# Kernel optimization log

Measured on AMD Instinct MI355X. Metric: run time of the kernel, lower is better.

The kernel has to match this reference:

```python
import jax, jax.numpy as jnp
import numpy as np

SIGMA = 20.0  # outlier threshold from FindOutliers


def setup_inputs() -> dict:
    key = jax.random.key(0)
    k1, k2, k3 = jax.random.split(key, 3)
    B, S, K, N = 4, 2048, 4096, 4096
    x = jax.random.normal(k1, (B, S, K), dtype=jnp.float32).astype(jnp.float16)
    # inject outlier columns (every 512th column scaled up) so |x| > sigma fires,
    # exercising the mixed sparse(outlier)/dense int8 decomposition
    x = (x.astype(jnp.float32).at[..., ::512].multiply(40.0)).astype(jnp.float16)
    weight = (jax.random.normal(k2, (N, K), dtype=jnp.float32) * 0.02).astype(jnp.float16)
    bias = (jax.random.normal(k3, (N,), dtype=jnp.float32) * 0.01).astype(jnp.float16)
    return {"x": x, "weight": weight, "bias": bias}


def reference(x, weight, bias):
    # x: [B, S, K] fp16; weight: [N, K] fp16; bias: [N] fp16
    B, S, K = x.shape
    N = weight.shape[0]
    xf = x.astype(jnp.float32).reshape(-1, K)            # [M, K]
    w32 = weight.astype(jnp.float32)                     # [N, K]

    # FindOutliers: columns of the flattened activation with any |value| > sigma
    out_mask = jnp.any(jnp.abs(xf) > SIGMA, axis=0)      # [K] bool

    # weight quantization: zero outlier columns, per-output-row symmetric int8 scale
    w_base = jnp.where(out_mask[None, :], 0.0, w32)      # [N, K]
    scale_col = (jnp.max(jnp.abs(w_base), axis=1) / 127.0).astype(jnp.float16).astype(jnp.float32)
    scale_col = jnp.maximum(scale_col, 1e-8)             # guard all-zero rows
    q_w = jnp.round(jnp.clip(w_base / scale_col[:, None], -128.0, 127.0)).astype(jnp.int8)

    # FindRowScaleF32: per-row symmetric int8 quantization of the activation
    scale_row = jnp.max(jnp.abs(xf), axis=1, keepdims=True) / 127.0   # [M, 1] fp32
    scale_row = jnp.maximum(scale_row, 1e-8)
    q_x = jnp.round(jnp.clip(xf / scale_row, -128.0, 127.0)).astype(jnp.int8)

    # int8 GEMM with int32 accumulation, fused dequant epilogue
    acc = jax.lax.dot_general(q_x, q_w, (((1,), (1,)), ((), ())),
                              preferred_element_type=jnp.int32)      # [M, N]
    y = acc.astype(jnp.float32) * scale_row * scale_col[None, :]

    # sparse outlier part in fp16-precision math: x[:, ind] @ weight[:, ind].T
    # (expressed as a masked dense GEMM for jit-static shapes; same math)
    y = y + (xf * out_mask[None, :]) @ (w32 * out_mask[None, :]).T

    y = y + bias.astype(jnp.float32)[None, :]
    return y.reshape(B, S, N).astype(jnp.float16)
```

## Files before the change

### kernel.cpp

```cpp
#include <hip/hip_runtime.h>
#include <hip/hip_fp16.h>
#include <stdint.h>

#define GAS __attribute__((address_space(1)))
#define LAS __attribute__((address_space(3)))

static constexpr int K_TOT = 4096;
static constexpr int N_TOT = 4096;
static constexpr int NO_CAP = 64;
static constexpr float SIGMA = 20.0f;

typedef int v4i __attribute__((ext_vector_type(4)));

__global__ __launch_bounds__(256) void k_init(int* __restrict__ mask) {
  mask[blockIdx.x * 256 + threadIdx.x] = 0;
}

__global__ __launch_bounds__(256) void k_quant_x(const float* __restrict__ x,
                                                 int8_t* __restrict__ qx,
                                                 float* __restrict__ scale_row,
                                                 int* __restrict__ mask) {
  const int lane = threadIdx.x & 63;
  const int wid  = threadIdx.x >> 6;
  const int m = blockIdx.x * 4 + wid;
  const float* xr = x + (size_t)m * K_TOT;

  float4 v[16];
  float amax = 0.0f;
#pragma unroll
  for (int it = 0; it < 16; ++it) {
    const int k0 = it * 256 + lane * 4;
    v[it] = *(const float4*)(xr + k0);
    const float a0 = fabsf(v[it].x), a1 = fabsf(v[it].y);
    const float a2 = fabsf(v[it].z), a3 = fabsf(v[it].w);
    amax = fmaxf(amax, fmaxf(fmaxf(a0, a1), fmaxf(a2, a3)));
    if (a0 > SIGMA) mask[k0 + 0] = 1;
    if (a1 > SIGMA) mask[k0 + 1] = 1;
    if (a2 > SIGMA) mask[k0 + 2] = 1;
    if (a3 > SIGMA) mask[k0 + 3] = 1;
  }
#pragma unroll
  for (int off = 32; off > 0; off >>= 1)
    amax = fmaxf(amax, __shfl_xor(amax, off));

  const float s = fmaxf(amax / 127.0f, 1e-8f);
  if (lane == 0) scale_row[m] = s;

  int8_t* qr = qx + (size_t)m * K_TOT;
#pragma unroll
  for (int it = 0; it < 16; ++it) {
    const int k0 = it * 256 + lane * 4;
    const int q0 = (int)rintf(fminf(fmaxf(v[it].x / s, -128.0f), 127.0f));
    const int q1 = (int)rintf(fminf(fmaxf(v[it].y / s, -128.0f), 127.0f));
    const int q2 = (int)rintf(fminf(fmaxf(v[it].z / s, -128.0f), 127.0f));
    const int q3 = (int)rintf(fminf(fmaxf(v[it].w / s, -128.0f), 127.0f));
    const uint32_t p = (uint32_t)(q0 & 0xFF) | ((uint32_t)(q1 & 0xFF) << 8) |
                       ((uint32_t)(q2 & 0xFF) << 16) | ((uint32_t)(q3 & 0xFF) << 24);
    *(uint32_t*)(qr + k0) = p;
  }
}

__global__ __launch_bounds__(256) void k_compact(const int* __restrict__ mask,
                                                 uint8_t* __restrict__ bitbytes,
                                                 int* __restrict__ ind,
                                                 int* __restrict__ count) {
  const int t = threadIdx.x;
  int local[16];
  int cnt = 0;
  uint32_t bits = 0;
#pragma unroll
  for (int j = 0; j < 16; ++j) {
    const int k = t * 16 + j;
    if (mask[k]) { bits |= (1u << j); local[cnt++] = k; }
  }
  bitbytes[2 * t]     = (uint8_t)(bits & 0xFF);
  bitbytes[2 * t + 1] = (uint8_t)((bits >> 8) & 0xFF);

  const int lane = t & 63, wid = t >> 6;
  int incl = cnt;
  for (int off = 1; off < 64; off <<= 1) {
    int o = __shfl_up(incl, off);
    if (lane >= off) incl += o;
  }
  __shared__ int wsum[4];
  if (lane == 63) wsum[wid] = incl;
  __syncthreads();
  int base = 0;
  for (int i = 0; i < wid; ++i) base += wsum[i];
  const int excl = base + incl - cnt;
  for (int j = 0; j < cnt; ++j) {
    const int pos = excl + j;
    if (pos < NO_CAP) ind[pos] = local[j];
  }
  if (t == 255) {
    const int tot = excl + cnt;
    *count = tot > NO_CAP ? NO_CAP : tot;
  }
}

__global__ __launch_bounds__(256) void k_quant_w(const float* __restrict__ w,
                                                 const uint8_t* __restrict__ bitbytes,
                                                 const int* __restrict__ ind,
                                                 const int* __restrict__ count,
                                                 int8_t* __restrict__ qw,
                                                 float* __restrict__ scale_col,
                                                 float* __restrict__ wo) {
  const int lane = threadIdx.x & 63;
  const int wid  = threadIdx.x >> 6;
  const int n = blockIdx.x * 4 + wid;
  const float* wr_ = w + (size_t)n * K_TOT;

  float4 v[16];
  float amax = 0.0f;
#pragma unroll
  for (int it = 0; it < 16; ++it) {
    const int k0 = it * 256 + lane * 4;
    v[it] = *(const float4*)(wr_ + k0);
    const uint32_t b = (uint32_t)(bitbytes[k0 >> 3] >> (k0 & 7));
    if (b & 1u) v[it].x = 0.0f;
    if (b & 2u) v[it].y = 0.0f;
    if (b & 4u) v[it].z = 0.0f;
    if (b & 8u) v[it].w = 0.0f;
    amax = fmaxf(amax, fmaxf(fmaxf(fabsf(v[it].x), fabsf(v[it].y)),
                             fmaxf(fabsf(v[it].z), fabsf(v[it].w))));
  }
#pragma unroll
  for (int off = 32; off > 0; off >>= 1)
    amax = fmaxf(amax, __shfl_xor(amax, off));

  float s = amax / 127.0f;
  s = __half2float(__float2half_rn(s));
  s = fmaxf(s, 1e-8f);
  if (lane == 0) scale_col[n] = s;

  int8_t* qr = qw + (size_t)n * K_TOT;
#pragma unroll
  for (int it = 0; it < 16; ++it) {
    const int k0 = it * 256 + lane * 4;
    const int q0 = (int)rintf(fminf(fmaxf(v[it].x / s, -128.0f), 127.0f));
    const int q1 = (int)rintf(fminf(fmaxf(v[it].y / s, -128.0f), 127.0f));
    const int q2 = (int)rintf(fminf(fmaxf(v[it].z / s, -128.0f), 127.0f));
    const int q3 = (int)rintf(fminf(fmaxf(v[it].w / s, -128.0f), 127.0f));
    const uint32_t p = (uint32_t)(q0 & 0xFF) | ((uint32_t)(q1 & 0xFF) << 8) |
                       ((uint32_t)(q2 & 0xFF) << 16) | ((uint32_t)(q3 & 0xFF) << 24);
    *(uint32_t*)(qr + k0) = p;
  }

  const int cnt = *count;
  if (lane < NO_CAP) {
    float val = 0.0f;
    if (lane < cnt) val = wr_[ind[lane]];
    wo[(size_t)n * NO_CAP + lane] = val;
  }
}

__global__ __launch_bounds__(256) void k_gather_xo(const float* __restrict__ x,
                                                   const int* __restrict__ ind,
                                                   const int* __restrict__ count,
                                                   float* __restrict__ xo) {
  const int idx = blockIdx.x * 256 + threadIdx.x;
  const int m = idx >> 6, j = idx & 63;
  const int cnt = *count;
  float val = 0.0f;
  if (j < cnt) val = x[(size_t)m * K_TOT + ind[j]];
  xo[(size_t)m * NO_CAP + j] = val;
}

#define STAGE_A(h, kt, bufb) do { \
  __builtin_amdgcn_global_load_lds((const GAS void*)(qx + gAoff[0] + (size_t)(h)*128*K_TOT + (size_t)(kt)*128), \
      (LAS void*)(smem + (bufb)*32768 + (h)*16384 + ldsOff0), 16, 0, 0); \
  __builtin_amdgcn_global_load_lds((const GAS void*)(qx + gAoff[1] + (size_t)(h)*128*K_TOT + (size_t)(kt)*128), \
      (LAS void*)(smem + (bufb)*32768 + (h)*16384 + ldsOff1), 16, 0, 0); \
} while (0)

#define STAGE_B(h, kt, bufb) do { \
  __builtin_amdgcn_global_load_lds((const GAS void*)(qw + gBoff[0] + (size_t)(h)*128*K_TOT + (size_t)(kt)*128), \
      (LAS void*)(smem + 65536 + (bufb)*32768 + (h)*16384 + ldsOff0), 16, 0, 0); \
  __builtin_amdgcn_global_load_lds((const GAS void*)(qw + gBoff[1] + (size_t)(h)*128*K_TOT + (size_t)(kt)*128), \
      (LAS void*)(smem + 65536 + (bufb)*32768 + (h)*16384 + ldsOff1), 16, 0, 0); \
} while (0)

#define LDA(mq, bufb) do { \
  _Pragma("unroll") for (int i_ = 0; i_ < 4; ++i_) \
  _Pragma("unroll") for (int ks_ = 0; ks_ < 2; ++ks_) \
    a[(mq)*4 + i_][ks_] = *(const v4i*)(smem + aHalfBase + (bufb)*32768 + ((mq)*4 + i_)*2048 + ks_*1024 + rcSwz); \
} while (0)

#define LDB(dst, nq, bufb) do { \
  _Pragma("unroll") for (int i_ = 0; i_ < 2; ++i_) \
  _Pragma("unroll") for (int ks_ = 0; ks_ < 2; ++ks_) \
    dst[i_][ks_] = *(const v4i*)(smem + bHalfBase + (bufb)*32768 + (bColBlk + (nq)*2 + i_)*2048 + ks_*1024 + rcSwz); \
} while (0)

#define MM(mq, nq, bsrc) do { \
  _Pragma("unroll") for (int i_ = 0; i_ < 4; ++i_) \
  _Pragma("unroll") for (int j_ = 0; j_ < 2; ++j_) \
  _Pragma("unroll") for (int ks_ = 0; ks_ < 2; ++ks_) \
    acc[(mq)*4 + i_][(nq)*2 + j_] = __builtin_amdgcn_mfma_i32_16x16x64_i8( \
        a[(mq)*4 + i_][ks_], bsrc[j_][ks_], acc[(mq)*4 + i_][(nq)*2 + j_], 0, 0, 0); \
} while (0)

#define BAR() __builtin_amdgcn_s_barrier()
#define PHASE_MFMA(mq, nq, bsrc) do { \
  BAR(); \
  __builtin_amdgcn_s_setprio(1); \
  MM(mq, nq, bsrc); \
  __builtin_amdgcn_s_setprio(0); \
} while (0)

__global__ __launch_bounds__(512, 2) void k_gemm8(const int8_t* __restrict__ qx,
                                                  const int8_t* __restrict__ qw,
                                                  const float* __restrict__ scale_row,
                                                  const float* __restrict__ scale_col,
                                                  const float* __restrict__ xo,
                                                  const float* __restrict__ wo,
                                                  const int* __restrict__ countp,
                                                  const float* __restrict__ bias,
                                                  float* __restrict__ out) {
  extern __shared__ int8_t smem[];
  constexpr int NT = K_TOT / 128;

  const int t = threadIdx.x;
  const int lane = t & 63;
  const int wid = t >> 6;
  const int wm = wid >> 2;
  const int wn = wid & 3;

  const int nbx = gridDim.x;
  const int nwg = gridDim.x * gridDim.y;
  int lin = blockIdx.y * nbx + blockIdx.x;
  lin = (lin & 7) * (nwg >> 3) + (lin >> 3);
  const int bm0 = (lin % nbx) * 256;
  const int bn0 = (lin / nbx) * 256;

  size_t gAoff[2], gBoff[2];
#pragma unroll
  for (int l = 0; l < 2; ++l) {
    const int f = l * 512 + t;
    const int rb = f >> 7, kb = (f >> 6) & 1, r = (f >> 2) & 15, c16 = f & 3;
    const int c16s = c16 ^ ((r & 8) ? 2 : 0);
    const int rowInHalf = rb * 16 + r;
    const int colByte = kb * 64 + c16s * 16;
    gAoff[l] = (size_t)(bm0 + rowInHalf) * K_TOT + colByte;
    gBoff[l] = (size_t)(bn0 + rowInHalf) * K_TOT + colByte;
  }
  const int ldsOff0 = wid * 1024;
  const int ldsOff1 = 8192 + wid * 1024;

  const int rr = lane & 15;
  const int rcSwz = rr * 64 + (((lane >> 4) * 16) ^ ((lane & 8) ? 32 : 0));
  const int aHalfBase = wm * 16384;
  const int bHalfBase = 65536 + (wn >> 1) * 16384;
  const int bColBlk = (wn & 1) * 4;

  v4i acc[8][4];
#pragma unroll
  for (int i = 0; i < 8; ++i)
#pragma unroll
    for (int j = 0; j < 4; ++j) acc[i][j] = (v4i){0, 0, 0, 0};
  v4i a[8][2], b0[2][2], b1[2][2];

  STAGE_A(0, 0, 0);
  STAGE_A(1, 0, 0);
  STAGE_B(0, 0, 0);
  STAGE_B(1, 0, 0);
  STAGE_A(0, 1, 1);
  STAGE_A(1, 1, 1);
  STAGE_B(0, 1, 1);
  STAGE_B(1, 1, 1);
  asm volatile("s_waitcnt vmcnt(8)" ::: "memory");
  BAR();

#pragma unroll 2
  for (int t0 = 0; t0 < NT; ++t0) {
    const int buf = t0 & 1;
    LDA(0, buf);
    LDB(b0, 0, buf);
    PHASE_MFMA(0, 0, b0);
    LDB(b1, 1, buf);
    LDA(1, buf);
    PHASE_MFMA(0, 1, b1);
    if (t0 + 2 < NT) {
      STAGE_A(0, t0 + 2, buf);
      STAGE_A(1, t0 + 2, buf);
    }
    PHASE_MFMA(1, 1, b1);
    if (t0 + 2 < NT) {
      STAGE_B(0, t0 + 2, buf);
      STAGE_B(1, t0 + 2, buf);
    }
    if (t0 < NT - 2) {
      asm volatile("s_waitcnt vmcnt(8)" ::: "memory");
    } else {
      asm volatile("s_waitcnt vmcnt(0)" ::: "memory");
    }
    PHASE_MFMA(1, 0, b0);
  }

  const int cnt = *countp;
  const int col = lane & 15;
  const int row4 = (lane >> 4) * 4;

  float scn[4], bzn[4];
  int nn[4];
#pragma unroll
  for (int ni = 0; ni < 4; ++ni) {
    const int n = bn0 + wn * 64 + ni * 16 + col;
    nn[ni] = n;
    scn[ni] = scale_col[n];
    bzn[ni] = bias[n];
  }

  if (cnt <= 8) {
    float wv[4][8];
#pragma unroll
    for (int ni = 0; ni < 4; ++ni)
#pragma unroll
      for (int j = 0; j < 8; ++j) wv[ni][j] = wo[(size_t)nn[ni] * NO_CAP + j];
#pragma unroll
    for (int mi = 0; mi < 8; ++mi) {
#pragma unroll
      for (int r = 0; r < 4; ++r) {
        const int m = bm0 + wm * 128 + mi * 16 + row4 + r;
        const float srm = scale_row[m];
        float xv[8];
#pragma unroll
        for (int j = 0; j < 8; ++j) xv[j] = xo[(size_t)m * NO_CAP + j];
#pragma unroll
        for (int ni = 0; ni < 4; ++ni) {
          float y = (float)acc[mi][ni][r] * srm * scn[ni];
#pragma unroll
          for (int j = 0; j < 8; ++j) y += xv[j] * wv[ni][j];
          y += bzn[ni];
          __builtin_nontemporal_store(__half2float(__float2half_rn(y)),
                                      &out[(size_t)m * N_TOT + nn[ni]]);
        }
      }
    }
  } else {
#pragma unroll
    for (int mi = 0; mi < 8; ++mi) {
#pragma unroll
      for (int r = 0; r < 4; ++r) {
        const int m = bm0 + wm * 128 + mi * 16 + row4 + r;
        const float srm = scale_row[m];
#pragma unroll
        for (int ni = 0; ni < 4; ++ni) {
          float y = (float)acc[mi][ni][r] * srm * scn[ni];
          for (int j = 0; j < cnt; ++j)
            y += xo[(size_t)m * NO_CAP + j] * wo[(size_t)nn[ni] * NO_CAP + j];
          y += bzn[ni];
          __builtin_nontemporal_store(__half2float(__float2half_rn(y)),
                                      &out[(size_t)m * N_TOT + nn[ni]]);
        }
      }
    }
  }
}

extern "C" void kernel_launch(void* const* d_in, const int* in_sizes, int n_in,
                              void* d_out, int out_size, void* d_ws, size_t ws_size,
                              hipStream_t stream) {
  const float* x    = (const float*)d_in[0];
  const float* w    = (const float*)d_in[1];
  const float* bias = (const float*)d_in[2];
  float* out        = (float*)d_out;

  const int M = in_sizes[0] / K_TOT;

  char* ws = (char*)d_ws;
  const size_t OFF_SR   = 0;
  const size_t OFF_SC   = OFF_SR + sizeof(float) * (size_t)M;
  const size_t OFF_MASK = OFF_SC + sizeof(float) * (size_t)N_TOT;
  const size_t OFF_IND  = OFF_MASK + sizeof(int) * (size_t)K_TOT;
  const size_t OFF_CNT  = OFF_IND + sizeof(int) * (size_t)NO_CAP;
  const size_t OFF_BB   = OFF_CNT + 256;
  const size_t OFF_XO   = (OFF_BB + (size_t)(K_TOT / 8) + 255) & ~(size_t)255;
  const size_t OFF_WO   = OFF_XO + sizeof(float) * (size_t)M * NO_CAP;
  const size_t OFF_QX   = (OFF_WO + sizeof(float) * (size_t)N_TOT * NO_CAP + 255) & ~(size_t)255;
  const size_t OFF_QW   = OFF_QX + (size_t)M * K_TOT;

  float* scale_row  = (float*)(ws + OFF_SR);
  float* scale_col  = (float*)(ws + OFF_SC);
  int* mask         = (int*)(ws + OFF_MASK);
  int* ind          = (int*)(ws + OFF_IND);
  int* count        = (int*)(ws + OFF_CNT);
  uint8_t* bitbytes = (uint8_t*)(ws + OFF_BB);
  float* xo         = (float*)(ws + OFF_XO);
  float* wo         = (float*)(ws + OFF_WO);
  int8_t* qx        = (int8_t*)(ws + OFF_QX);
  int8_t* qw        = (int8_t*)(ws + OFF_QW);

  hipFuncSetAttribute((const void*)k_gemm8,
                      hipFuncAttributeMaxDynamicSharedMemorySize, 131072);

  hipLaunchKernelGGL(k_init, dim3(K_TOT / 256), dim3(256), 0, stream, mask);
  hipLaunchKernelGGL(k_quant_x, dim3(M / 4), dim3(256), 0, stream, x, qx, scale_row, mask);
  hipLaunchKernelGGL(k_compact, dim3(1), dim3(256), 0, stream, mask, bitbytes, ind, count);
  hipLaunchKernelGGL(k_quant_w, dim3(N_TOT / 4), dim3(256), 0, stream,
                     w, bitbytes, ind, count, qw, scale_col, wo);
  hipLaunchKernelGGL(k_gather_xo, dim3((M * NO_CAP) / 256), dim3(256), 0, stream, x, ind, count, xo);
  hipLaunchKernelGGL(k_gemm8, dim3(M / 256, N_TOT / 256), dim3(512), 131072, stream,
                     qx, qw, scale_row, scale_col, xo, wo, count, bias, out);
}
```

Baseline: 230.6 us.

## Merge weight quant with outlier gather, memset mask, regroup GEMM tile order

Result: faster. 223.7 us, median of 2 (-3.0%).

```diff
diff --git a/kernel.cpp b/kernel.cpp
--- a/kernel.cpp
+++ b/kernel.cpp
@@ -11,10 +11,6 @@
 static constexpr float SIGMA = 20.0f;
 
 typedef int v4i __attribute__((ext_vector_type(4)));
-
-__global__ __launch_bounds__(256) void k_init(int* __restrict__ mask) {
-  mask[blockIdx.x * 256 + threadIdx.x] = 0;
-}
 
 __global__ __launch_bounds__(256) void k_quant_x(const float* __restrict__ x,
                                                  int8_t* __restrict__ qx,
@@ -98,13 +94,25 @@
   }
 }
 
-__global__ __launch_bounds__(256) void k_quant_w(const float* __restrict__ w,
-                                                 const uint8_t* __restrict__ bitbytes,
-                                                 const int* __restrict__ ind,
-                                                 const int* __restrict__ count,
-                                                 int8_t* __restrict__ qw,
-                                                 float* __restrict__ scale_col,
-                                                 float* __restrict__ wo) {
+__global__ __launch_bounds__(256) void k_quant_w_gather(const float* __restrict__ w,
+                                                        const float* __restrict__ x,
+                                                        const uint8_t* __restrict__ bitbytes,
+                                                        const int* __restrict__ ind,
+                                                        const int* __restrict__ count,
+                                                        int8_t* __restrict__ qw,
+                                                        float* __restrict__ scale_col,
+                                                        float* __restrict__ wo,
+                                                        float* __restrict__ xo,
+                                                        int nwb) {
+  if ((int)blockIdx.x >= nwb) {
+    const int idx = (blockIdx.x - nwb) * 256 + threadIdx.x;
+    const int m = idx >> 6, j = idx & 63;
+    const int cnt = *count;
+    float val = 0.0f;
+    if (j < cnt) val = x[(size_t)m * K_TOT + ind[j]];
+    xo[(size_t)m * NO_CAP + j] = val;
+    return;
+  }
   const int lane = threadIdx.x & 63;
   const int wid  = threadIdx.x >> 6;
   const int n = blockIdx.x * 4 + wid;
@@ -152,18 +160,6 @@
     if (lane < cnt) val = wr_[ind[lane]];
     wo[(size_t)n * NO_CAP + lane] = val;
   }
-}
-
-__global__ __launch_bounds__(256) void k_gather_xo(const float* __restrict__ x,
-                                                   const int* __restrict__ ind,
-                                                   const int* __restrict__ count,
-                                                   float* __restrict__ xo) {
-  const int idx = blockIdx.x * 256 + threadIdx.x;
-  const int m = idx >> 6, j = idx & 63;
-  const int cnt = *count;
-  float val = 0.0f;
-  if (j < cnt) val = x[(size_t)m * K_TOT + ind[j]];
-  xo[(size_t)m * NO_CAP + j] = val;
 }
 
 #define STAGE_A(h, kt, bufb) do { \
@@ -227,19 +223,19 @@
   const int wn = wid & 3;
 
   const int nbx = gridDim.x;
-  const int nwg = gridDim.x * gridDim.y;
-  int lin = blockIdx.y * nbx + blockIdx.x;
-  lin = (lin & 7) * (nwg >> 3) + (lin >> 3);
-  const int bm0 = (lin % nbx) * 256;
-  const int bn0 = (lin / nbx) * 256;
+  const int o = blockIdx.y * nbx + blockIdx.x;
+  const int gm_cnt = nbx >> 3;
+  const int g = o >> 6, r = o & 63;
+  const int bm0 = (((g % gm_cnt) << 3) + (r & 7)) * 256;
+  const int bn0 = (((g / gm_cnt) << 3) + (r >> 3)) * 256;
 
   size_t gAoff[2], gBoff[2];
 #pragma unroll
   for (int l = 0; l < 2; ++l) {
     const int f = l * 512 + t;
-    const int rb = f >> 7, kb = (f >> 6) & 1, r = (f >> 2) & 15, c16 = f & 3;
-    const int c16s = c16 ^ ((r & 8) ? 2 : 0);
-    const int rowInHalf = rb * 16 + r;
+    const int rb = f >> 7, kb = (f >> 6) & 1, rr_ = (f >> 2) & 15, c16 = f & 3;
+    const int c16s = c16 ^ ((rr_ & 8) ? 2 : 0);
+    const int rowInHalf = rb * 16 + rr_;
     const int colByte = kb * 64 + c16s * 16;
     gAoff[l] = (size_t)(bm0 + rowInHalf) * K_TOT + colByte;
     gBoff[l] = (size_t)(bn0 + rowInHalf) * K_TOT + colByte;
@@ -320,15 +316,15 @@
 #pragma unroll
     for (int mi = 0; mi < 8; ++mi) {
 #pragma unroll
-      for (int r = 0; r < 4; ++r) {
-        const int m = bm0 + wm * 128 + mi * 16 + row4 + r;
+      for (int r2 = 0; r2 < 4; ++r2) {
+        const int m = bm0 + wm * 128 + mi * 16 + row4 + r2;
         const float srm = scale_row[m];
         float xv[8];
 #pragma unroll
         for (int j = 0; j < 8; ++j) xv[j] = xo[(size_t)m * NO_CAP + j];
 #pragma unroll
         for (int ni = 0; ni < 4; ++ni) {
-          float y = (float)acc[mi][ni][r] * srm * scn[ni];
+          float y = (float)acc[mi][ni][r2] * srm * scn[ni];
 #pragma unroll
           for (int j = 0; j < 8; ++j) y += xv[j] * wv[ni][j];
           y += bzn[ni];
@@ -341,12 +337,12 @@
 #pragma unroll
     for (int mi = 0; mi < 8; ++mi) {
 #pragma unroll
-      for (int r = 0; r < 4; ++r) {
-        const int m = bm0 + wm * 128 + mi * 16 + row4 + r;
+      for (int r2 = 0; r2 < 4; ++r2) {
+        const int m = bm0 + wm * 128 + mi * 16 + row4 + r2;
         const float srm = scale_row[m];
 #pragma unroll
         for (int ni = 0; ni < 4; ++ni) {
-          float y = (float)acc[mi][ni][r] * srm * scn[ni];
+          float y = (float)acc[mi][ni][r2] * srm * scn[ni];
           for (int j = 0; j < cnt; ++j)
             y += xo[(size_t)m * NO_CAP + j] * wo[(size_t)nn[ni] * NO_CAP + j];
           y += bzn[ni];
@@ -394,12 +390,13 @@
   hipFuncSetAttribute((const void*)k_gemm8,
                       hipFuncAttributeMaxDynamicSharedMemorySize, 131072);
 
-  hipLaunchKernelGGL(k_init, dim3(K_TOT / 256), dim3(256), 0, stream, mask);
+  hipMemsetAsync(mask, 0, sizeof(int) * (size_t)K_TOT, stream);
   hipLaunchKernelGGL(k_quant_x, dim3(M / 4), dim3(256), 0, stream, x, qx, scale_row, mask);
   hipLaunchKernelGGL(k_compact, dim3(1), dim3(256), 0, stream, mask, bitbytes, ind, count);
-  hipLaunchKernelGGL(k_quant_w, dim3(N_TOT / 4), dim3(256), 0, stream,
-                     w, bitbytes, ind, count, qw, scale_col, wo);
-  hipLaunchKernelGGL(k_gather_xo, dim3((M * NO_CAP) / 256), dim3(256), 0, stream, x, ind, count, xo);
+  const int nwb = N_TOT / 4;
+  const int ngb = (M * NO_CAP) / 256;
+  hipLaunchKernelGGL(k_quant_w_gather, dim3(nwb + ngb), dim3(256), 0, stream,
+                     w, x, bitbytes, ind, count, qw, scale_col, wo, xo, nwb);
   hipLaunchKernelGGL(k_gemm8, dim3(M / 256, N_TOT / 256), dim3(512), 131072, stream,
                      qx, qw, scale_row, scale_col, xo, wo, count, bias, out);
 }
```
